# Optimization experiments

Measured on AMD Instinct MI355X. Metric: run time of the kernel, lower is better.

The kernel has to match this reference:

```python
import jax, jax.numpy as jnp
import numpy as np

D_MODEL = 1024
H = 16
D_K = D_MODEL // H  # 64
B, S = 2, 2048


def setup_inputs() -> dict:
    key = jax.random.key(0)
    ks = jax.random.split(key, 8)
    scale = 1.0 / np.sqrt(D_MODEL)
    return {
        "q": jax.random.normal(ks[0], (B, S, D_MODEL), dtype=jnp.float32),
        "k": jax.random.normal(ks[1], (B, S, D_MODEL), dtype=jnp.float32),
        "v": jax.random.normal(ks[2], (B, S, D_MODEL), dtype=jnp.float32),
        "W_q": jax.random.normal(ks[3], (H, D_MODEL, D_K), dtype=jnp.float32) * scale,
        "W_k": jax.random.normal(ks[4], (H, D_MODEL, D_K), dtype=jnp.float32) * scale,
        "W_v": jax.random.normal(ks[5], (H, D_MODEL, D_K), dtype=jnp.float32) * scale,
        "W_o": jax.random.normal(ks[6], (D_MODEL, H * D_K), dtype=jnp.float32) * scale,
        "b_o": jnp.zeros((D_MODEL,), dtype=jnp.float32),
    }


def reference(q, k, v, W_q, W_k, W_v, W_o, b_o):
    b, s, _ = q.shape
    h, _, d_k = W_q.shape
    inv_sqrt_dk = jnp.asarray(1.0 / np.sqrt(d_k), q.dtype)
    # per-head projections: [b, h, s, d_k]
    qh = jnp.einsum("bsd,hdk->bhsk", q, W_q)
    kh = jnp.einsum("bsd,hdk->bhsk", k, W_k)
    vh = jnp.einsum("bsd,hdk->bhsk", v, W_v)
    # scaled dot product attention
    scores = jnp.einsum("bhqk,bhsk->bhqs", qh, kh) * inv_sqrt_dk  # [b,h,S,S]
    attn = jax.nn.softmax(scores, axis=-1)
    ctx = jnp.einsum("bhqs,bhsk->bhqk", attn, vh)  # [b,h,S,d_k]
    # chunk over heads + concat along feature dim -> [b, S, h*d_k], head-major
    ctx = ctx.transpose(0, 2, 1, 3).reshape(b, s, h * d_k)
    # final linear
    return ctx @ W_o.T + b_o
```

## Files before the change

kernel.cpp:

```cpp
#include <hip/hip_runtime.h>
#include <cstdint>
#include <cstddef>


typedef unsigned short bf16_t;
typedef __attribute__((ext_vector_type(8))) short short8;
typedef __attribute__((ext_vector_type(4))) float f32x4;

__device__ __forceinline__ uint32_t fbits(float f) {
  union { float f; uint32_t u; } v; v.f = f; return v.u;
}
__device__ __forceinline__ bf16_t f2bf(float f) {
  uint32_t u = fbits(f);
  return (bf16_t)((u + 0x7FFFu + ((u >> 16) & 1u)) >> 16);
}
__device__ __forceinline__ uint32_t packbf2(float lo, float hi) {
  uint32_t a = fbits(hi) + 0x8000u;
  uint32_t b = fbits(lo) + 0x8000u;
  return __builtin_amdgcn_perm(a, b, 0x07060302u);
}

__global__ void prep_kernel(const float* __restrict__ q, const float* __restrict__ k,
                            const float* __restrict__ v, const float* __restrict__ Wo,
                            const float* __restrict__ Wq, const float* __restrict__ Wk,
                            const float* __restrict__ Wv,
                            bf16_t* __restrict__ qo, bf16_t* __restrict__ ko,
                            bf16_t* __restrict__ vo, bf16_t* __restrict__ Woo,
                            bf16_t* __restrict__ Wtq, bf16_t* __restrict__ Wtk,
                            bf16_t* __restrict__ Wtv) {
  int blk = blockIdx.x;
  int tid = threadIdx.x;
  if (blk < 13312) {
    const float* src; bf16_t* dst; int i;
    if (blk < 4096)       { src = q;  dst = qo;  i = blk * 256 + tid; }
    else if (blk < 8192)  { src = k;  dst = ko;  i = (blk - 4096) * 256 + tid; }
    else if (blk < 12288) { src = v;  dst = vo;  i = (blk - 8192) * 256 + tid; }
    else                  { src = Wo; dst = Woo; i = (blk - 12288) * 256 + tid; }
    f32x4 val = ((const f32x4*)src)[i];
    ushort4 o;
    o.x = f2bf(val.x); o.y = f2bf(val.y); o.z = f2bf(val.z); o.w = f2bf(val.w);
    ((ushort4*)dst)[i] = o;
  } else {
    int blk2 = blk - 13312;
    int z = blk2 >> 9, t = blk2 & 511;
    const float* W = z == 0 ? Wq : z == 1 ? Wk : Wv;
    bf16_t* Wt = z == 0 ? Wtq : z == 1 ? Wtk : Wtv;
    int h = t >> 5, d0 = (t & 31) * 32;
    __shared__ float tile[32][65];
    const float* src = W + ((size_t)h << 16) + (size_t)d0 * 64;
    int d = tid >> 3;
#pragma unroll
    for (int j = 0; j < 2; j++) {
      int dk = (tid & 7) * 8 + j * 4;
      *(f32x4*)&tile[d][dk] = *(const f32x4*)(src + d * 64 + dk);
    }
    __syncthreads();
    int dk2 = tid >> 2, c = tid & 3;
    union { ushort s[8]; int4 v; } o;
#pragma unroll
    for (int j = 0; j < 8; j++) o.s[j] = f2bf(tile[c * 8 + j][dk2]);
    *(int4*)(Wt + (size_t)(h * 64 + dk2) * 1024 + d0 + c * 8) = o.v;
  }
}

__global__ __launch_bounds__(256) void gemm_proj_kernel(
    const bf16_t* __restrict__ A0, const bf16_t* __restrict__ A1, const bf16_t* __restrict__ A2,
    const bf16_t* __restrict__ B0, const bf16_t* __restrict__ B1, const bf16_t* __restrict__ B2,
    bf16_t* __restrict__ O0, bf16_t* __restrict__ O1, bf16_t* __restrict__ O2,
    float s0)
{
  const int z = blockIdx.z;
  const bf16_t* A  = z == 0 ? A0 : z == 1 ? A1 : A2;
  const bf16_t* Bt = z == 0 ? B0 : z == 1 ? B1 : B2;
  bf16_t* Cout     = z == 0 ? O0 : z == 1 ? O1 : O2;
  const float scale = z == 0 ? s0 : 1.0f;
  const int K = 1024;

  __shared__ alignas(16) bf16_t smem[18432];

  const int tid = threadIdx.x;
  const int lane = tid & 63, wave = tid >> 6;
  const int wm = wave >> 1, wn = wave & 1;
  const int quad = lane >> 4, l15 = lane & 15;
  const int m0 = blockIdx.y * 128, n0 = blockIdx.x * 128;

  f32x4 acc[4][4];
#pragma unroll
  for (int i = 0; i < 4; i++)
#pragma unroll
    for (int j = 0; j < 4; j++) acc[i][j] = (f32x4)0.0f;

  const int c0 = wave * 128 + lane;
  const int c1 = c0 + 64;
  const bf16_t* pa0 = A  + (size_t)(m0 + (c0 >> 2)) * K + (c0 & 3) * 8;
  const bf16_t* pa1 = A  + (size_t)(m0 + (c1 >> 2)) * K + (c1 & 3) * 8;
  const bf16_t* pb0 = Bt + (size_t)(n0 + (c0 >> 2)) * K + (c0 & 3) * 8;
  const bf16_t* pb1 = Bt + (size_t)(n0 + (c1 >> 2)) * K + (c1 & 3) * 8;
  const int s0a = c0 * 8, s1a = c1 * 8;

  int4 ra0 = *(const int4*)pa0;
  int4 ra1 = *(const int4*)pa1;
  int4 rb0 = *(const int4*)pb0;
  int4 rb1 = *(const int4*)pb1;
  *(int4*)(smem + s0a) = ra0;
  *(int4*)(smem + s1a) = ra1;
  *(int4*)(smem + 4096 + s0a) = rb0;
  *(int4*)(smem + 4096 + s1a) = rb1;
  __syncthreads();

  for (int it = 0; it < 32; ++it) {
    const int co = (it & 1) * 8192;
    if (it < 31) {
      const int ko = (it + 1) * 32;
      ra0 = *(const int4*)(pa0 + ko);
      ra1 = *(const int4*)(pa1 + ko);
      rb0 = *(const int4*)(pb0 + ko);
      rb1 = *(const int4*)(pb1 + ko);
    }

    short8 af[4], bfr[4];
#pragma unroll
    for (int mi = 0; mi < 4; mi++)
      af[mi] = *(const short8*)(smem + co + (wm * 64 + mi * 16 + l15) * 32 + quad * 8);
#pragma unroll
    for (int ni = 0; ni < 4; ni++)
      bfr[ni] = *(const short8*)(smem + co + 4096 + (wn * 64 + ni * 16 + l15) * 32 + quad * 8);
#pragma unroll
    for (int mi = 0; mi < 4; mi++)
#pragma unroll
      for (int ni = 0; ni < 4; ni++)
        acc[mi][ni] = __builtin_amdgcn_mfma_f32_16x16x32_bf16(af[mi], bfr[ni], acc[mi][ni], 0, 0, 0);

    if (it < 31) {
      const int no = ((it + 1) & 1) * 8192;
      *(int4*)(smem + no + s0a) = ra0;
      *(int4*)(smem + no + s1a) = ra1;
      *(int4*)(smem + no + 4096 + s0a) = rb0;
      *(int4*)(smem + no + 4096 + s1a) = rb1;
    }
    __syncthreads();
  }

  const int s0r = m0 & 2047, bb = m0 >> 11, hp = n0 >> 6;
  if (z < 2) {
    bf16_t* slot = smem + wn * 9216;
#pragma unroll
    for (int ni = 0; ni < 4; ni++)
#pragma unroll
      for (int mi = 0; mi < 4; mi++)
#pragma unroll
        for (int r = 0; r < 4; r++)
          slot[(wm * 64 + mi * 16 + quad * 4 + r) * 72 + ni * 16 + l15] =
              f2bf(acc[mi][ni][r] * scale);
    __syncthreads();
#pragma unroll
    for (int rd = 0; rd < 8; ++rd) {
      int idx = rd * 256 + tid;
      int si = idx >> 10, mm = (idx >> 3) & 127, c8 = idx & 7;
      int4 val = *(const int4*)(smem + si * 9216 + mm * 72 + c8 * 8);
      *(int4*)(Cout + ((size_t)((bb * 16 + hp + si) * 2048 + s0r + mm)) * 64 + c8 * 8) = val;
    }
  } else {
    bf16_t* slot = smem + wn * 8704;
#pragma unroll
    for (int ni = 0; ni < 4; ni++)
#pragma unroll
      for (int mi = 0; mi < 4; mi++) {
        uint2 pk = make_uint2(packbf2(acc[mi][ni][0], acc[mi][ni][1]),
                              packbf2(acc[mi][ni][2], acc[mi][ni][3]));
        *(uint2*)(slot + (ni * 16 + l15) * 136 + wm * 64 + mi * 16 + quad * 4) = pk;
      }
    __syncthreads();
#pragma unroll
    for (int rd = 0; rd < 8; ++rd) {
      int idx = rd * 256 + tid;
      int si = idx >> 10, c = (idx >> 4) & 63, ck = idx & 15;
      int4 val = *(const int4*)(smem + si * 8704 + c * 136 + ck * 8);
      *(int4*)(Cout + (size_t)(bb * 16 + hp + si) * 131072 + (size_t)c * 2048 + s0r + ck * 8) = val;
    }
  }
}

__global__ __launch_bounds__(256) void gemm_out_kernel(
    const bf16_t* __restrict__ A, const bf16_t* __restrict__ Bt,
    float* __restrict__ C, const float* __restrict__ bias)
{
  const int K = 1024, N = 1024;
  __shared__ alignas(16) bf16_t smem[12288];
  const int tid = threadIdx.x;
  const int lane = tid & 63, wave = tid >> 6;
  const int quad = lane >> 4, l15 = lane & 15;
  const int m0 = blockIdx.y * 128, n0 = blockIdx.x * 64;

  f32x4 acc[2][4];
#pragma unroll
  for (int i = 0; i < 2; i++)
#pragma unroll
    for (int j = 0; j < 4; j++) acc[i][j] = (f32x4)0.0f;

  const int c0 = wave * 128 + lane, c1 = c0 + 64;
  const int cb = wave * 64 + lane;
  const bf16_t* pa0 = A  + (size_t)(m0 + (c0 >> 2)) * K + (c0 & 3) * 8;
  const bf16_t* pa1 = A  + (size_t)(m0 + (c1 >> 2)) * K + (c1 & 3) * 8;
  const bf16_t* pb  = Bt + (size_t)(n0 + (cb >> 2)) * K + (cb & 3) * 8;
  const int s0a = c0 * 8, s1a = c1 * 8, sba = cb * 8;

  int4 ra0 = *(const int4*)pa0;
  int4 ra1 = *(const int4*)pa1;
  int4 rb  = *(const int4*)pb;
  *(int4*)(smem + s0a) = ra0;
  *(int4*)(smem + s1a) = ra1;
  *(int4*)(smem + 4096 + sba) = rb;
  __syncthreads();

  for (int it = 0; it < 32; ++it) {
    const int co = (it & 1) * 6144;
    if (it < 31) {
      const int ko = (it + 1) * 32;
      ra0 = *(const int4*)(pa0 + ko);
      ra1 = *(const int4*)(pa1 + ko);
      rb  = *(const int4*)(pb + ko);
    }

    short8 af[2], bfr[4];
#pragma unroll
    for (int mi = 0; mi < 2; mi++)
      af[mi] = *(const short8*)(smem + co + (wave * 32 + mi * 16 + l15) * 32 + quad * 8);
#pragma unroll
    for (int ni = 0; ni < 4; ni++)
      bfr[ni] = *(const short8*)(smem + co + 4096 + (ni * 16 + l15) * 32 + quad * 8);
#pragma unroll
    for (int mi = 0; mi < 2; mi++)
#pragma unroll
      for (int ni = 0; ni < 4; ni++)
        acc[mi][ni] = __builtin_amdgcn_mfma_f32_16x16x32_bf16(af[mi], bfr[ni], acc[mi][ni], 0, 0, 0);

    if (it < 31) {
      const int no = ((it + 1) & 1) * 6144;
      *(int4*)(smem + no + s0a) = ra0;
      *(int4*)(smem + no + s1a) = ra1;
      *(int4*)(smem + no + 4096 + sba) = rb;
    }
    __syncthreads();
  }

#pragma unroll
  for (int ni = 0; ni < 4; ni++) {
    int col = n0 + ni * 16 + l15;
    float bv = bias[col];
#pragma unroll
    for (int mi = 0; mi < 2; mi++) {
      int row = m0 + wave * 32 + mi * 16 + quad * 4;
#pragma unroll
      for (int r = 0; r < 4; r++)
        C[(size_t)(row + r) * N + col] = acc[mi][ni][r] + bv;
    }
  }
}

__global__ __launch_bounds__(512) void flash_kernel(
    const bf16_t* __restrict__ qh, const bf16_t* __restrict__ kh,
    const bf16_t* __restrict__ vT, bf16_t* __restrict__ ctx)
{
  __shared__ alignas(16) bf16_t KtF[2][4096];
  __shared__ alignas(16) bf16_t VtF[2][4096];
  __shared__ alignas(16) bf16_t PtF[16384];
  const int tid = threadIdx.x, lane = tid & 63, wave = tid >> 6;
  const int quad = lane >> 4, l15 = lane & 15;
  const int q0 = blockIdx.x * 256;
  const int h = blockIdx.y, b = blockIdx.z;
  const size_t headoff = (size_t)(b * 16 + h) * 2048 * 64;
  const bf16_t* Q = qh + headoff;
  const bf16_t* K = kh + headoff;
  const bf16_t* V = vT + headoff;

  short8 qf[2][2];
#pragma unroll
  for (int g = 0; g < 2; g++)
#pragma unroll
    for (int ks = 0; ks < 2; ks++)
      qf[g][ks] = *(const short8*)(Q + (size_t)(q0 + wave * 32 + g * 16 + l15) * 64
                                   + ks * 32 + quad * 8);

  f32x4 O[2][4];
#pragma unroll
  for (int g = 0; g < 2; g++)
#pragma unroll
    for (int mi = 0; mi < 4; mi++) O[g][mi] = (f32x4)0.0f;
  f32x4 lacc[2] = {(f32x4)0.0f, (f32x4)0.0f};

  const bf16_t* Kp = K + (size_t)((wave >> 1) * 16 + l15) * 64 + (wave & 1) * 32 + quad * 8;
  const bf16_t* Vp = V + (size_t)((wave >> 1) * 16 + l15) * 2048 + (wave & 1) * 32 + quad * 8;
  const int soff = wave * 512 + lane * 8;

  const int pwb = wave * 4096 + ((quad >> 1) * 16 + l15) * 16 + 8 * (quad & 1);

  int4 kreg = *(const int4*)Kp;
  int4 vreg = *(const int4*)Vp;
  *(int4*)(&KtF[0][soff]) = kreg;
  *(int4*)(&VtF[0][soff]) = vreg;
  __syncthreads();

  for (int it = 0; it < 32; ++it) {
    const int cur = it & 1, nxt = cur ^ 1;
    if (it < 31) {
      kreg = *(const int4*)(Kp + (size_t)(it + 1) * 4096);
      vreg = *(const int4*)(Vp + (it + 1) * 64);
    }

    f32x4 S[2][4];
#pragma unroll
    for (int g = 0; g < 2; g++)
#pragma unroll
      for (int mi = 0; mi < 4; mi++) S[g][mi] = (f32x4)0.0f;
#pragma unroll
    for (int ks = 0; ks < 2; ks++) {
#pragma unroll
      for (int mi = 0; mi < 4; mi++) {
        short8 kf = *(const short8*)(&KtF[cur][(mi * 2 + ks) * 512 + lane * 8]);
        S[0][mi] = __builtin_amdgcn_mfma_f32_16x16x32_bf16(kf, qf[0][ks], S[0][mi], 0, 0, 0);
        S[1][mi] = __builtin_amdgcn_mfma_f32_16x16x32_bf16(kf, qf[1][ks], S[1][mi], 0, 0, 0);
      }
    }

#pragma unroll
    for (int g = 0; g < 2; g++) {
#pragma unroll
      for (int mi = 0; mi < 4; mi++)
#pragma unroll
        for (int r = 0; r < 4; r++)
          S[g][mi][r] = __builtin_amdgcn_exp2f(S[g][mi][r]);
      lacc[g] += (S[g][0] + S[g][1]) + (S[g][2] + S[g][3]);
    }

#pragma unroll
    for (int g = 0; g < 2; g++)
#pragma unroll
      for (int mi = 0; mi < 4; mi++) {
        uint2 pk = make_uint2(packbf2(S[g][mi][0], S[g][mi][1]),
                              packbf2(S[g][mi][2], S[g][mi][3]));
        *(uint2*)((char*)PtF + pwb + g * 2048 + (mi >> 1) * 1024 + (mi & 1) * 512) = pk;
      }

#pragma unroll
    for (int ks = 0; ks < 2; ks++) {
      short8 pf0 = *(const short8*)(&PtF[wave * 2048 + (ks * 64 + lane) * 8]);
      short8 pf1 = *(const short8*)(&PtF[wave * 2048 + 1024 + (ks * 64 + lane) * 8]);
#pragma unroll
      for (int mi = 0; mi < 4; mi++) {
        short8 vf = *(const short8*)(&VtF[cur][(mi * 2 + ks) * 512 + lane * 8]);
        O[0][mi] = __builtin_amdgcn_mfma_f32_16x16x32_bf16(vf, pf0, O[0][mi], 0, 0, 0);
        O[1][mi] = __builtin_amdgcn_mfma_f32_16x16x32_bf16(vf, pf1, O[1][mi], 0, 0, 0);
      }
    }

    if (it < 31) {
      *(int4*)(&KtF[nxt][soff]) = kreg;
      *(int4*)(&VtF[nxt][soff]) = vreg;
    }
    __syncthreads();
  }

#pragma unroll
  for (int g = 0; g < 2; g++) {
    float l = (lacc[g][0] + lacc[g][1]) + (lacc[g][2] + lacc[g][3]);
    l += __shfl_xor(l, 16, 64);
    l += __shfl_xor(l, 32, 64);
    float inv = 1.0f / l;
    int qrow = q0 + wave * 32 + g * 16 + l15;
    bf16_t* crow = ctx + ((size_t)(b * 2048 + qrow)) * 1024 + h * 64;
#pragma unroll
    for (int mi = 0; mi < 4; mi++) {
      uint2 pk = make_uint2(packbf2(O[g][mi][0] * inv, O[g][mi][1] * inv),
                            packbf2(O[g][mi][2] * inv, O[g][mi][3] * inv));
      *(uint2*)(crow + mi * 16 + quad * 4) = pk;
    }
  }
}

extern "C" void kernel_launch(void* const* d_in, const int* in_sizes, int n_in,
                              void* d_out, int out_size, void* d_ws, size_t ws_size,
                              hipStream_t stream)
{
  const float* q  = (const float*)d_in[0];
  const float* k  = (const float*)d_in[1];
  const float* v  = (const float*)d_in[2];
  const float* Wq = (const float*)d_in[3];
  const float* Wk = (const float*)d_in[4];
  const float* Wv = (const float*)d_in[5];
  const float* Wo = (const float*)d_in[6];
  const float* bo = (const float*)d_in[7];
  float* out = (float*)d_out;

  const size_t NX = (size_t)4096 * 1024;
  const size_t NW = (size_t)1024 * 1024;

  char* p = (char*)d_ws;
  bf16_t* qbf = (bf16_t*)p; p += NX * 2;
  bf16_t* kbf = (bf16_t*)p; p += NX * 2;
  bf16_t* vbf = (bf16_t*)p; p += NX * 2;
  bf16_t* Wtq = (bf16_t*)p; p += NW * 2;
  bf16_t* Wtk = (bf16_t*)p; p += NW * 2;
  bf16_t* Wtv = (bf16_t*)p; p += NW * 2;
  bf16_t* Wob = (bf16_t*)p; p += NW * 2;
  bf16_t* qhb = (bf16_t*)p; p += NX * 2;
  bf16_t* khb = (bf16_t*)p; p += NX * 2;
  bf16_t* vTb = (bf16_t*)p; p += NX * 2;
  bf16_t* ctxb = (bf16_t*)p; p += NX * 2;

  prep_kernel<<<14848, 256, 0, stream>>>(q, k, v, Wo, Wq, Wk, Wv,
                                         qbf, kbf, vbf, Wob, Wtq, Wtk, Wtv);

  const float qscale = 0.125f * 1.44269504088896340736f;
  gemm_proj_kernel<<<dim3(8, 32, 3), 256, 0, stream>>>(qbf, kbf, vbf, Wtq, Wtk, Wtv,
                                                       qhb, khb, vTb, qscale);

  flash_kernel<<<dim3(8, 16, 2), 512, 0, stream>>>(qhb, khb, vTb, ctxb);

  gemm_out_kernel<<<dim3(16, 32), 256, 0, stream>>>(ctxb, Wob, out, bo);

  (void)in_sizes; (void)n_in; (void)out_size; (void)ws_size;
}
```

Baseline: 218.3 us.

## Fuse fp32-to-bf16 input conversion into projection GEMM loads and unroll flash loop

Removes the q/k/v conversion pass from the prep kernel; the projection GEMM now loads fp32 activations and packs them to bf16 before writing shared memory. This avoids writing and re-reading bf16 copies of the inputs, at the cost of doubled A-operand global traffic inside the GEMM. The flash attention loop is also manually unrolled by two with constant buffer indices and reorganized prefetch of K/V tiles.

```diff
diff --git a/kernel.cpp b/kernel.cpp
--- a/kernel.cpp
+++ b/kernel.cpp
@@ -19,29 +19,27 @@
   uint32_t b = fbits(lo) + 0x8000u;
   return __builtin_amdgcn_perm(a, b, 0x07060302u);
 }
-
-__global__ void prep_kernel(const float* __restrict__ q, const float* __restrict__ k,
-                            const float* __restrict__ v, const float* __restrict__ Wo,
+__device__ __forceinline__ int4 cvt8(f32x4 lo, f32x4 hi) {
+  return make_int4((int)packbf2(lo.x, lo.y), (int)packbf2(lo.z, lo.w),
+                   (int)packbf2(hi.x, hi.y), (int)packbf2(hi.z, hi.w));
+}
+
+__global__ void prep_kernel(const float* __restrict__ Wo,
                             const float* __restrict__ Wq, const float* __restrict__ Wk,
                             const float* __restrict__ Wv,
-                            bf16_t* __restrict__ qo, bf16_t* __restrict__ ko,
-                            bf16_t* __restrict__ vo, bf16_t* __restrict__ Woo,
+                            bf16_t* __restrict__ Woo,
                             bf16_t* __restrict__ Wtq, bf16_t* __restrict__ Wtk,
                             bf16_t* __restrict__ Wtv) {
   int blk = blockIdx.x;
   int tid = threadIdx.x;
-  if (blk < 13312) {
-    const float* src; bf16_t* dst; int i;
-    if (blk < 4096)       { src = q;  dst = qo;  i = blk * 256 + tid; }
-    else if (blk < 8192)  { src = k;  dst = ko;  i = (blk - 4096) * 256 + tid; }
-    else if (blk < 12288) { src = v;  dst = vo;  i = (blk - 8192) * 256 + tid; }
-    else                  { src = Wo; dst = Woo; i = (blk - 12288) * 256 + tid; }
-    f32x4 val = ((const f32x4*)src)[i];
+  if (blk < 1024) {
+    int i = blk * 256 + tid;
+    f32x4 val = ((const f32x4*)Wo)[i];
     ushort4 o;
     o.x = f2bf(val.x); o.y = f2bf(val.y); o.z = f2bf(val.z); o.w = f2bf(val.w);
-    ((ushort4*)dst)[i] = o;
+    ((ushort4*)Woo)[i] = o;
   } else {
-    int blk2 = blk - 13312;
+    int blk2 = blk - 1024;
     int z = blk2 >> 9, t = blk2 & 511;
     const float* W = z == 0 ? Wq : z == 1 ? Wk : Wv;
     bf16_t* Wt = z == 0 ? Wtq : z == 1 ? Wtk : Wtv;
@@ -64,13 +62,13 @@
 }
 
 __global__ __launch_bounds__(256) void gemm_proj_kernel(
-    const bf16_t* __restrict__ A0, const bf16_t* __restrict__ A1, const bf16_t* __restrict__ A2,
+    const float* __restrict__ A0, const float* __restrict__ A1, const float* __restrict__ A2,
     const bf16_t* __restrict__ B0, const bf16_t* __restrict__ B1, const bf16_t* __restrict__ B2,
     bf16_t* __restrict__ O0, bf16_t* __restrict__ O1, bf16_t* __restrict__ O2,
     float s0)
 {
   const int z = blockIdx.z;
-  const bf16_t* A  = z == 0 ? A0 : z == 1 ? A1 : A2;
+  const float* A   = z == 0 ? A0 : z == 1 ? A1 : A2;
   const bf16_t* Bt = z == 0 ? B0 : z == 1 ? B1 : B2;
   bf16_t* Cout     = z == 0 ? O0 : z == 1 ? O1 : O2;
   const float scale = z == 0 ? s0 : 1.0f;
@@ -92,18 +90,18 @@
 
   const int c0 = wave * 128 + lane;
   const int c1 = c0 + 64;
-  const bf16_t* pa0 = A  + (size_t)(m0 + (c0 >> 2)) * K + (c0 & 3) * 8;
-  const bf16_t* pa1 = A  + (size_t)(m0 + (c1 >> 2)) * K + (c1 & 3) * 8;
+  const float*  pa0 = A  + (size_t)(m0 + (c0 >> 2)) * K + (c0 & 3) * 8;
+  const float*  pa1 = A  + (size_t)(m0 + (c1 >> 2)) * K + (c1 & 3) * 8;
   const bf16_t* pb0 = Bt + (size_t)(n0 + (c0 >> 2)) * K + (c0 & 3) * 8;
   const bf16_t* pb1 = Bt + (size_t)(n0 + (c1 >> 2)) * K + (c1 & 3) * 8;
   const int s0a = c0 * 8, s1a = c1 * 8;
 
-  int4 ra0 = *(const int4*)pa0;
-  int4 ra1 = *(const int4*)pa1;
+  f32x4 ra0l = *(const f32x4*)pa0, ra0h = *(const f32x4*)(pa0 + 4);
+  f32x4 ra1l = *(const f32x4*)pa1, ra1h = *(const f32x4*)(pa1 + 4);
   int4 rb0 = *(const int4*)pb0;
   int4 rb1 = *(const int4*)pb1;
-  *(int4*)(smem + s0a) = ra0;
-  *(int4*)(smem + s1a) = ra1;
+  *(int4*)(smem + s0a) = cvt8(ra0l, ra0h);
+  *(int4*)(smem + s1a) = cvt8(ra1l, ra1h);
   *(int4*)(smem + 4096 + s0a) = rb0;
   *(int4*)(smem + 4096 + s1a) = rb1;
   __syncthreads();
@@ -112,8 +110,8 @@
     const int co = (it & 1) * 8192;
     if (it < 31) {
       const int ko = (it + 1) * 32;
-      ra0 = *(const int4*)(pa0 + ko);
-      ra1 = *(const int4*)(pa1 + ko);
+      ra0l = *(const f32x4*)(pa0 + ko); ra0h = *(const f32x4*)(pa0 + ko + 4);
+      ra1l = *(const f32x4*)(pa1 + ko); ra1h = *(const f32x4*)(pa1 + ko + 4);
       rb0 = *(const int4*)(pb0 + ko);
       rb1 = *(const int4*)(pb1 + ko);
     }
@@ -133,8 +131,8 @@
 
     if (it < 31) {
       const int no = ((it + 1) & 1) * 8192;
-      *(int4*)(smem + no + s0a) = ra0;
-      *(int4*)(smem + no + s1a) = ra1;
+      *(int4*)(smem + no + s0a) = cvt8(ra0l, ra0h);
+      *(int4*)(smem + no + s1a) = cvt8(ra1l, ra1h);
       *(int4*)(smem + no + 4096 + s0a) = rb0;
       *(int4*)(smem + no + 4096 + s1a) = rb1;
     }
@@ -292,22 +290,9 @@
   const bf16_t* Kp = K + (size_t)((wave >> 1) * 16 + l15) * 64 + (wave & 1) * 32 + quad * 8;
   const bf16_t* Vp = V + (size_t)((wave >> 1) * 16 + l15) * 2048 + (wave & 1) * 32 + quad * 8;
   const int soff = wave * 512 + lane * 8;
-
   const int pwb = wave * 4096 + ((quad >> 1) * 16 + l15) * 16 + 8 * (quad & 1);
 
-  int4 kreg = *(const int4*)Kp;
-  int4 vreg = *(const int4*)Vp;
-  *(int4*)(&KtF[0][soff]) = kreg;
-  *(int4*)(&VtF[0][soff]) = vreg;
-  __syncthreads();
-
-  for (int it = 0; it < 32; ++it) {
-    const int cur = it & 1, nxt = cur ^ 1;
-    if (it < 31) {
-      kreg = *(const int4*)(Kp + (size_t)(it + 1) * 4096);
-      vreg = *(const int4*)(Vp + (it + 1) * 64);
-    }
-
+  auto body = [&](int buf) {
     f32x4 S[2][4];
 #pragma unroll
     for (int g = 0; g < 2; g++)
@@ -317,12 +302,11 @@
     for (int ks = 0; ks < 2; ks++) {
 #pragma unroll
       for (int mi = 0; mi < 4; mi++) {
-        short8 kf = *(const short8*)(&KtF[cur][(mi * 2 + ks) * 512 + lane * 8]);
+        short8 kf = *(const short8*)(&KtF[buf][(mi * 2 + ks) * 512 + lane * 8]);
         S[0][mi] = __builtin_amdgcn_mfma_f32_16x16x32_bf16(kf, qf[0][ks], S[0][mi], 0, 0, 0);
         S[1][mi] = __builtin_amdgcn_mfma_f32_16x16x32_bf16(kf, qf[1][ks], S[1][mi], 0, 0, 0);
       }
     }
-
 #pragma unroll
     for (int g = 0; g < 2; g++) {
 #pragma unroll
@@ -332,7 +316,6 @@
           S[g][mi][r] = __builtin_amdgcn_exp2f(S[g][mi][r]);
       lacc[g] += (S[g][0] + S[g][1]) + (S[g][2] + S[g][3]);
     }
-
 #pragma unroll
     for (int g = 0; g < 2; g++)
 #pragma unroll
@@ -341,23 +324,45 @@
                               packbf2(S[g][mi][2], S[g][mi][3]));
         *(uint2*)((char*)PtF + pwb + g * 2048 + (mi >> 1) * 1024 + (mi & 1) * 512) = pk;
       }
-
 #pragma unroll
     for (int ks = 0; ks < 2; ks++) {
       short8 pf0 = *(const short8*)(&PtF[wave * 2048 + (ks * 64 + lane) * 8]);
       short8 pf1 = *(const short8*)(&PtF[wave * 2048 + 1024 + (ks * 64 + lane) * 8]);
 #pragma unroll
       for (int mi = 0; mi < 4; mi++) {
-        short8 vf = *(const short8*)(&VtF[cur][(mi * 2 + ks) * 512 + lane * 8]);
+        short8 vf = *(const short8*)(&VtF[buf][(mi * 2 + ks) * 512 + lane * 8]);
         O[0][mi] = __builtin_amdgcn_mfma_f32_16x16x32_bf16(vf, pf0, O[0][mi], 0, 0, 0);
         O[1][mi] = __builtin_amdgcn_mfma_f32_16x16x32_bf16(vf, pf1, O[1][mi], 0, 0, 0);
       }
     }
-
-    if (it < 31) {
-      *(int4*)(&KtF[nxt][soff]) = kreg;
-      *(int4*)(&VtF[nxt][soff]) = vreg;
-    }
+  };
+
+  int4 k0 = *(const int4*)Kp, v0 = *(const int4*)Vp;
+  *(int4*)(&KtF[0][soff]) = k0;
+  *(int4*)(&VtF[0][soff]) = v0;
+  int4 kA = *(const int4*)(Kp + 4096), vA = *(const int4*)(Vp + 64);
+  __syncthreads();
+
+  for (int it = 0; it < 32; it += 2) {
+    *(int4*)(&KtF[1][soff]) = kA;
+    *(int4*)(&VtF[1][soff]) = vA;
+    int4 kB, vB;
+    if (it + 2 < 32) {
+      kB = *(const int4*)(Kp + (size_t)(it + 2) * 4096);
+      vB = *(const int4*)(Vp + (size_t)(it + 2) * 64);
+    }
+    body(0);
+    __syncthreads();
+
+    if (it + 2 < 32) {
+      *(int4*)(&KtF[0][soff]) = kB;
+      *(int4*)(&VtF[0][soff]) = vB;
+    }
+    if (it + 3 < 32) {
+      kA = *(const int4*)(Kp + (size_t)(it + 3) * 4096);
+      vA = *(const int4*)(Vp + (size_t)(it + 3) * 64);
+    }
+    body(1);
     __syncthreads();
   }
 
@@ -396,9 +401,6 @@
   const size_t NW = (size_t)1024 * 1024;
 
   char* p = (char*)d_ws;
-  bf16_t* qbf = (bf16_t*)p; p += NX * 2;
-  bf16_t* kbf = (bf16_t*)p; p += NX * 2;
-  bf16_t* vbf = (bf16_t*)p; p += NX * 2;
   bf16_t* Wtq = (bf16_t*)p; p += NW * 2;
   bf16_t* Wtk = (bf16_t*)p; p += NW * 2;
   bf16_t* Wtv = (bf16_t*)p; p += NW * 2;
@@ -408,11 +410,10 @@
   bf16_t* vTb = (bf16_t*)p; p += NX * 2;
   bf16_t* ctxb = (bf16_t*)p; p += NX * 2;
 
-  prep_kernel<<<14848, 256, 0, stream>>>(q, k, v, Wo, Wq, Wk, Wv,
-                                         qbf, kbf, vbf, Wob, Wtq, Wtk, Wtv);
+  prep_kernel<<<2560, 256, 0, stream>>>(Wo, Wq, Wk, Wv, Wob, Wtq, Wtk, Wtv);
 
   const float qscale = 0.125f * 1.44269504088896340736f;
-  gemm_proj_kernel<<<dim3(8, 32, 3), 256, 0, stream>>>(qbf, kbf, vbf, Wtq, Wtk, Wtv,
+  gemm_proj_kernel<<<dim3(8, 32, 3), 256, 0, stream>>>(q, k, v, Wtq, Wtk, Wtv,
                                                        qhb, khb, vTb, qscale);
 
   flash_kernel<<<dim3(8, 16, 2), 512, 0, stream>>>(qhb, khb, vTb, ctxb);
```

New measurement: 228.9 us. +4.8%, slower.
